# Performance work log

Measured on AMD Instinct MI355X. Metric: run time of the kernel, lower is better.

## Reference

```python
import jax, jax.numpy as jnp
import numpy as np

NUM_HEADS = 12
WS = 8
ROPE_BASE = 100.0  # croco/dust3r RoPE2D default frequency base


def _rope1d(t, p, inv_freq):
    # t: [Bw, h, N, d], p: [Bw, N], inv_freq: [d/2]
    freqs = p[..., None] * inv_freq                      # [Bw, N, d/2]
    emb = jnp.concatenate([freqs, freqs], axis=-1)       # [Bw, N, d]
    cos = jnp.cos(emb)[:, None, :, :]
    sin = jnp.sin(emb)[:, None, :, :]
    t1, t2 = jnp.split(t, 2, axis=-1)
    rot = jnp.concatenate([-t2, t1], axis=-1)            # rotate_half
    return t * cos + rot * sin


def _rope2d(tokens, pos):
    # tokens: [Bw, h, N, D], pos: [Bw, N, 2] (y, x). First D/2 dims use y, last D/2 use x.
    D = tokens.shape[-1]
    d = D // 2
    inv_freq = 1.0 / (ROPE_BASE ** (jnp.arange(0, d, 2, dtype=jnp.float32) / d))
    ty, tx = jnp.split(tokens, 2, axis=-1)
    return jnp.concatenate([_rope1d(ty, pos[..., 0], inv_freq),
                            _rope1d(tx, pos[..., 1], inv_freq)], axis=-1)


def setup_inputs() -> dict:
    B, H, W, C = 16, 64, 64, 768
    key = jax.random.key(0)
    ks = jax.random.split(key, 7)
    x_img = jax.random.normal(ks[0], (B, H * W, C), dtype=jnp.float32)
    yy, xx = jnp.meshgrid(jnp.arange(H), jnp.arange(W), indexing='ij')
    pos = jnp.stack([yy, xx], axis=-1).reshape(1, H * W, 2).astype(jnp.float32)
    pos2d_img = jnp.broadcast_to(pos, (B, H * W, 2))
    unseen = jax.random.normal(ks[1], (B, C), dtype=jnp.float32)
    sc = C ** -0.5
    qkv_w = jax.random.normal(ks[2], (3 * C, C), dtype=jnp.float32) * sc
    qkv_b = jax.random.normal(ks[3], (3 * C,), dtype=jnp.float32) * 0.02
    proj_w = jax.random.normal(ks[4], (C, C), dtype=jnp.float32) * sc
    proj_b = jax.random.normal(ks[5], (C,), dtype=jnp.float32) * 0.02
    return {'x_img': x_img, 'pos2d_img': pos2d_img, 'unseen': unseen,
            'qkv_w': qkv_w, 'qkv_b': qkv_b, 'proj_w': proj_w, 'proj_b': proj_b,
            'H': H, 'W': W}


def reference(x_img, pos2d_img, unseen, qkv_w, qkv_b, proj_w, proj_b, H, W):
    B, HW, C = x_img.shape
    hd = C // NUM_HEADS
    scale = hd ** -0.5
    nWh, nWw = H // WS, W // WS
    Bwin, Nwin = B * nWh * nWw, WS * WS

    # window partition
    xw = x_img.reshape(B, nWh, WS, nWw, WS, C).transpose(0, 1, 3, 2, 4, 5).reshape(Bwin, Nwin, C)
    pw = pos2d_img.reshape(B, nWh, WS, nWw, WS, 2).transpose(0, 1, 3, 2, 4, 5).reshape(Bwin, Nwin, 2)

    # append unseen token (shared across windows of an image)
    u = jnp.broadcast_to(unseen[:, None, None, :], (B, nWh * nWw, 1, C)).reshape(Bwin, 1, C)
    xw = jnp.concatenate([xw, u], axis=1)                # [Bwin, Nwin+1, C]

    qkv = xw @ qkv_w.T + qkv_b                           # [Bwin, N, 3C]
    qkv = qkv.reshape(Bwin, Nwin + 1, 3, NUM_HEADS, hd)
    q = qkv[:, :, 0].transpose(0, 2, 1, 3)               # [Bwin, h, N, hd]
    k = qkv[:, :, 1].transpose(0, 2, 1, 3)
    v = qkv[:, :, 2].transpose(0, 2, 1, 3)

    # RoPE2D on image tokens only; unseen token gets no RoPE
    q = jnp.concatenate([_rope2d(q[:, :, :Nwin], pw), q[:, :, Nwin:]], axis=2)
    k = jnp.concatenate([_rope2d(k[:, :, :Nwin], pw), k[:, :, Nwin:]], axis=2)

    attn = jax.nn.softmax(jnp.einsum('bhqd,bhkd->bhqk', q, k) * scale, axis=-1)
    out = jnp.einsum('bhqk,bhkd->bhqd', attn, v)
    out = out.transpose(0, 2, 1, 3).reshape(Bwin, Nwin + 1, C)
    out = out @ proj_w.T + proj_b

    # window merge
    out_img = out[:, :Nwin].reshape(B, nWh, nWw, WS, WS, C).transpose(0, 1, 3, 2, 4, 5).reshape(B, HW, C)
    out_unseen = out[:, Nwin].reshape(B, nWh * nWw, C).mean(axis=1)  # [B, C]
    return out_img, out_unseen
```

## Files before the change

kernel.cpp:

```cpp
#include <hip/hip_runtime.h>
#include <cstdint>
#include <cstddef>

typedef __attribute__((ext_vector_type(8)))  __bf16 bf16x8;
typedef __attribute__((ext_vector_type(4)))  float  f32x4;
typedef __attribute__((ext_vector_type(2)))  unsigned int u32x2;
typedef __attribute__((ext_vector_type(4)))  unsigned int u32x4;

#define DI __device__ __forceinline__

constexpr int Cdim = 768;
constexpr int C3   = 2304;
constexpr int NT   = 65;
constexpr int ROWS = 1024 * NT;
constexpr int ROWS_PAD = ROWS + 32;
constexpr int TP   = 96;
constexpr int PS   = 128;
constexpr long long OUT_IMG = 16LL * 4096 * 768;

DI float bf2f(unsigned short u) { unsigned int x = (unsigned int)u << 16; float f; __builtin_memcpy(&f, &x, 4); return f; }
DI unsigned short f2bf(float f) { unsigned int x; __builtin_memcpy(&x, &f, 4); x = x + 0x7fffu + ((x >> 16) & 1u); return (unsigned short)(x >> 16); }

DI void gload_lds16(const unsigned short* g, unsigned short* l) {
  __builtin_amdgcn_global_load_lds((__attribute__((address_space(1))) void*)g,
                                   (__attribute__((address_space(3))) void*)l, 16, 0, 0);
}

__global__ void k_prep(const float* __restrict__ qkv_w, const float* __restrict__ proj_w,
                       unsigned short* __restrict__ wqb, unsigned short* __restrict__ wpb,
                       float* __restrict__ rope) {
  const int NW1 = 2304 * 768;
  const int NW2 = 768 * 768;
  int total = NW1 + NW2 + 1024;
  for (int i = blockIdx.x * blockDim.x + threadIdx.x; i < total; i += gridDim.x * blockDim.x) {
    if (i < NW1) wqb[i] = f2bf(qkv_w[i]);
    else if (i < NW1 + NW2) wpb[i - NW1] = f2bf(proj_w[i - NW1]);
    else {
      int e = i - NW1 - NW2;
      int p = e >> 4, j = e & 15;
      float inv = powf(100.f, -(float)j * (1.f / 16.f));
      float a = (float)p * inv;
      rope[2 * e]     = cosf(a);
      rope[2 * e + 1] = sinf(a);
    }
  }
}

__global__ void k_xw(const float* __restrict__ x, const float* __restrict__ unseen,
                     unsigned short* __restrict__ xw) {
  int row = blockIdx.x;
  int w = row / NT, t = row - w * NT;
  const float* src;
  if (t == 64) {
    src = unseen + (size_t)(w >> 6) * Cdim;
  } else {
    int wy = (w >> 3) & 7, wx = w & 7;
    int hw = ((wy << 3) + (t >> 3)) * 64 + (wx << 3) + (t & 7);
    src = x + ((size_t)(w >> 6) * 4096 + hw) * Cdim;
  }
  float4 v = ((const float4*)src)[threadIdx.x];
  unsigned int u0 = (unsigned)f2bf(v.x) | ((unsigned)f2bf(v.y) << 16);
  unsigned int u1 = (unsigned)f2bf(v.z) | ((unsigned)f2bf(v.w) << 16);
  ((u32x2*)(xw + (size_t)row * Cdim))[threadIdx.x] = (u32x2){u0, u1};
}

template<int MODE, int NTILES>
__global__ __launch_bounds__(256, 4) void k_gemm(
    const unsigned short* __restrict__ A, const unsigned short* __restrict__ Bw,
    const float* __restrict__ bias, const float* __restrict__ rope,
    unsigned short* __restrict__ Cb, float* __restrict__ outp) {
  constexpr int K = 768;
  __shared__ alignas(16) unsigned short As[128 * 64];
  __shared__ alignas(16) unsigned short Bs[128 * 64];

  constexpr int nwg = 520 * NTILES;
  constexpr int q8 = nwg / 8, r8 = nwg % 8;
  int id = blockIdx.x;
  int xcd = id & 7, lid = id >> 3;
  int wg = (xcd < r8 ? xcd * (q8 + 1) : r8 * (q8 + 1) + (xcd - r8) * q8) + lid;
  int mtile = wg / NTILES, ntile = wg - mtile * NTILES;
  int m0 = mtile * 128, n0 = ntile * 128;

  int tid = threadIdx.x;
  int lane = tid & 63, wid = tid >> 6;
  int lq = lane & 15, lg = lane >> 4;
  int wm = (wid >> 1) * 64;
  int wn = (wid & 1) * 64;

  f32x4 acc[4][4];
  #pragma unroll
  for (int i = 0; i < 4; ++i)
    #pragma unroll
    for (int j = 0; j < 4; ++j) acc[i][j] = (f32x4){0.f, 0.f, 0.f, 0.f};

  for (int kt = 0; kt < K / 64; ++kt) {
    int k0 = kt * 64;
    #pragma unroll
    for (int c = 0; c < 4; ++c) {
      int chunk = c * 256 + tid;
      int row = chunk >> 3, kc = chunk & 7;
      int skc = kc ^ (row & 7);
      gload_lds16(A + (size_t)(m0 + row) * K + k0 + skc * 8,
                  As + (size_t)(c * 256 + (tid & ~63)) * 8);
    }
    #pragma unroll
    for (int c = 0; c < 4; ++c) {
      int chunk = c * 256 + tid;
      int row = chunk >> 3, kc = chunk & 7;
      int skc = kc ^ (row & 7);
      gload_lds16(Bw + (size_t)(n0 + row) * K + k0 + skc * 8,
                  Bs + (size_t)(c * 256 + (tid & ~63)) * 8);
    }
    asm volatile("s_waitcnt vmcnt(0)" ::: "memory");
    __syncthreads();
    #pragma unroll
    for (int ks = 0; ks < 2; ++ks) {
      bf16x8 af[4], bfr[4];
      #pragma unroll
      for (int mt = 0; mt < 4; ++mt) {
        int row = wm + mt * 16 + lq;
        int ch = ((ks << 2) + lg) ^ (row & 7);
        af[mt] = *(const bf16x8*)(As + row * 64 + ch * 8);
      }
      #pragma unroll
      for (int nt = 0; nt < 4; ++nt) {
        int row = wn + nt * 16 + lq;
        int ch = ((ks << 2) + lg) ^ (row & 7);
        bfr[nt] = *(const bf16x8*)(Bs + row * 64 + ch * 8);
      }
      #pragma unroll
      for (int mt = 0; mt < 4; ++mt)
        #pragma unroll
        for (int nt = 0; nt < 4; ++nt)
          acc[mt][nt] = __builtin_amdgcn_mfma_f32_16x16x32_bf16(af[mt], bfr[nt], acc[mt][nt], 0, 0, 0);
    }
    __syncthreads();
  }

  if (MODE == 0) {
    unsigned short* ct = As;
    #pragma unroll
    for (int mt = 0; mt < 4; ++mt) {
      #pragma unroll
      for (int r = 0; r < 4; ++r) {
        int lrow = wm + mt * 16 + (lg << 2) + r;
        int grow = m0 + lrow;
        int w = grow / NT, t = grow - w * NT;
        int wy = (w >> 3) & 7, wx = w & 7;
        int py = (wy << 3) + (t >> 3), px = (wx << 3) + (t & 7);
        #pragma unroll
        for (int a = 0; a < 2; ++a) {
          int cn0 = wn + a * 32 + lq;
          int col0 = n0 + cn0, col1 = col0 + 16;
          float v0 = acc[mt][2 * a][r] + bias[col0];
          float v1 = acc[mt][2 * a + 1][r] + bias[col1];
          if (col0 < 1536 && t != 64) {
            int p = a ? px : py;
            const float* rp = rope + ((p << 4) + lq) * 2;
            float cc = rp[0], ss = rp[1];
            float o0 = v0 * cc - v1 * ss;
            float o1 = v1 * cc + v0 * ss;
            v0 = o0; v1 = o1;
          }
          int b0 = (lrow * 256 + cn0 * 2) ^ ((lrow & 7) << 4);
          int b1 = (lrow * 256 + (cn0 + 16) * 2) ^ ((lrow & 7) << 4);
          *(unsigned short*)((char*)ct + b0) = f2bf(v0);
          *(unsigned short*)((char*)ct + b1) = f2bf(v1);
        }
      }
    }
    __syncthreads();
    #pragma unroll
    for (int j = 0; j < 8; ++j) {
      int idx = j * 256 + tid;
      int row = idx >> 4, c = idx & 15;
      u32x4 v = *(const u32x4*)((char*)ct + row * 256 + ((c ^ (row & 7)) << 4));
      *(u32x4*)(Cb + (size_t)(m0 + row) * C3 + n0 + c * 8) = v;
    }
  } else {
    float* cf = (float*)As;
    #pragma unroll
    for (int half = 0; half < 2; ++half) {
      if ((wm >> 6) == half) {
        #pragma unroll
        for (int mt = 0; mt < 4; ++mt) {
          #pragma unroll
          for (int r = 0; r < 4; ++r) {
            int lrow = mt * 16 + (lg << 2) + r;
            int grow = m0 + half * 64 + lrow;
            int w = grow / NT, t = grow - w * NT;
            #pragma unroll
            for (int a = 0; a < 2; ++a) {
              int cn0 = wn + a * 32 + lq;
              int col0 = n0 + cn0, col1 = col0 + 16;
              float v0 = acc[mt][2 * a][r] + bias[col0];
              float v1 = acc[mt][2 * a + 1][r] + bias[col1];
              if (t == 64) {
                float* ub = outp + OUT_IMG + (size_t)(w >> 6) * Cdim;
                atomicAdd(ub + col0, v0 * (1.f / 64.f));
                atomicAdd(ub + col1, v1 * (1.f / 64.f));
              } else {
                int b0 = (lrow * 512 + cn0 * 4) ^ ((lrow & 7) << 4);
                int b1 = (lrow * 512 + (cn0 + 16) * 4) ^ ((lrow & 7) << 4);
                *(float*)((char*)cf + b0) = v0;
                *(float*)((char*)cf + b1) = v1;
              }
            }
          }
        }
      }
      __syncthreads();
      #pragma unroll
      for (int j = 0; j < 8; ++j) {
        int idx = j * 256 + tid;
        int row = idx >> 5, c = idx & 31;
        int grow = m0 + half * 64 + row;
        int w = grow / NT, t = grow - w * NT;
        if (t != 64) {
          int wy = (w >> 3) & 7, wx = w & 7;
          int py = (wy << 3) + (t >> 3), px = (wx << 3) + (t & 7);
          u32x4 v = *(const u32x4*)((char*)cf + row * 512 + ((c ^ (row & 7)) << 4));
          *(u32x4*)(outp + ((size_t)(w >> 6) * 4096 + py * 64 + px) * Cdim + n0 + c * 4) = v;
        }
      }
      __syncthreads();
    }
  }
}

__global__ void k_vt(const unsigned short* __restrict__ qkv, unsigned short* __restrict__ Vt) {
  int bh = blockIdx.x;
  int w = bh / 12, h = bh - w * 12;
  __shared__ float sv[65][65];
  const unsigned short* base = qkv + (size_t)w * NT * C3 + 1536 + h * 64;
  for (int i = threadIdx.x; i < 65 * 64; i += 256) {
    int t = i >> 6, d = i & 63;
    sv[t][d] = bf2f(base[(size_t)t * C3 + d]);
  }
  __syncthreads();
  unsigned short* out = Vt + (size_t)bh * 64 * TP;
  for (int i = threadIdx.x; i < 64 * (TP / 8); i += 256) {
    int d = i / (TP / 8), tc = i - d * (TP / 8);
    int t0 = tc * 8;
    unsigned int u[4];
    #pragma unroll
    for (int k = 0; k < 4; ++k) {
      int ta = t0 + 2 * k, tb = ta + 1;
      unsigned short sa = (ta < 65) ? f2bf(sv[ta][d]) : (unsigned short)0;
      unsigned short sb = (tb < 65) ? f2bf(sv[tb][d]) : (unsigned short)0;
      u[k] = (unsigned)sa | ((unsigned)sb << 16);
    }
    *(u32x4*)(out + d * TP + t0) = (u32x4){u[0], u[1], u[2], u[3]};
  }
}

__global__ __launch_bounds__(64) void k_attn(const unsigned short* __restrict__ qkv,
                                             const unsigned short* __restrict__ Vt,
                                             unsigned short* __restrict__ att) {
  __shared__ alignas(16) unsigned short P[80 * PS];
  int h = blockIdx.x, w = blockIdx.y;
  int lane = threadIdx.x;
  int lq = lane & 15, lg = lane >> 4;

  const unsigned short* qb = qkv + (size_t)w * NT * C3 + h * 64;
  const unsigned short* kb = qb + 768;

  bf16x8 kf[5][2];
  #pragma unroll
  for (int kt = 0; kt < 5; ++kt)
    #pragma unroll
    for (int ks = 0; ks < 2; ++ks)
      kf[kt][ks] = *(const bf16x8*)(kb + (size_t)(kt * 16 + lq) * C3 + ks * 32 + lg * 8);

  const unsigned short* vb = Vt + (size_t)(w * 12 + h) * 64 * TP;
  bf16x8 vf[3][4];
  #pragma unroll
  for (int ks = 0; ks < 3; ++ks)
    #pragma unroll
    for (int dt = 0; dt < 4; ++dt)
      vf[ks][dt] = *(const bf16x8*)(vb + (size_t)(dt * 16 + lq) * TP + ks * 32 + lg * 8);

  for (int i = lane; i < 80 * 8; i += 64) {
    int row = i >> 3, j = i & 7;
    int byteo = row * (PS * 2) + 160 + j * 4;
    byteo ^= (row & 7) << 4;
    *(unsigned int*)((char*)P + byteo) = 0u;
  }

  #pragma unroll 1
  for (int qt = 0; qt < 5; ++qt) {
    bf16x8 qf[2];
    #pragma unroll
    for (int ks = 0; ks < 2; ++ks)
      qf[ks] = *(const bf16x8*)(qb + (size_t)(qt * 16 + lq) * C3 + ks * 32 + lg * 8);

    f32x4 sa[5];
    #pragma unroll
    for (int kt = 0; kt < 5; ++kt) {
      sa[kt] = (f32x4){0.f, 0.f, 0.f, 0.f};
      #pragma unroll
      for (int ks = 0; ks < 2; ++ks)
        sa[kt] = __builtin_amdgcn_mfma_f32_16x16x32_bf16(kf[kt][ks], qf[ks], sa[kt], 0, 0, 0);
    }
    float pv[5][4];
    float m = -1e30f;
    #pragma unroll
    for (int kt = 0; kt < 5; ++kt)
      #pragma unroll
      for (int r = 0; r < 4; ++r) {
        int tok = kt * 16 + lg * 4 + r;
        float s = sa[kt][r] * 0.125f;
        bool ok = tok < 65;
        pv[kt][r] = ok ? s : -1e30f;
        m = (ok && s > m) ? s : m;
      }
    m = fmaxf(m, __shfl_xor(m, 16));
    m = fmaxf(m, __shfl_xor(m, 32));
    float sum = 0.f;
    #pragma unroll
    for (int kt = 0; kt < 5; ++kt)
      #pragma unroll
      for (int r = 0; r < 4; ++r) {
        float e = (pv[kt][r] > -1e29f) ? exp2f((pv[kt][r] - m) * 1.44269504f) : 0.f;
        pv[kt][r] = e;
        sum += e;
      }
    sum += __shfl_xor(sum, 16);
    sum += __shfl_xor(sum, 32);
    float rinv = 1.f / sum;

    int q = qt * 16 + lq;
    #pragma unroll
    for (int kt = 0; kt < 5; ++kt) {
      unsigned int u0 = (unsigned)f2bf(pv[kt][0] * rinv) | ((unsigned)f2bf(pv[kt][1] * rinv) << 16);
      unsigned int u1 = (unsigned)f2bf(pv[kt][2] * rinv) | ((unsigned)f2bf(pv[kt][3] * rinv) << 16);
      int byteo = q * (PS * 2) + kt * 32 + lg * 8;
      byteo ^= (q & 7) << 4;
      *(u32x2*)((char*)P + byteo) = (u32x2){u0, u1};
    }
    asm volatile("s_waitcnt lgkmcnt(0)" ::: "memory");

    bf16x8 bp[3];
    #pragma unroll
    for (int ks = 0; ks < 3; ++ks) {
      int byteo = q * (PS * 2) + ks * 64 + lg * 16;
      byteo ^= (q & 7) << 4;
      bp[ks] = *(const bf16x8*)((char*)P + byteo);
    }
    #pragma unroll
    for (int dt = 0; dt < 4; ++dt) {
      f32x4 o = (f32x4){0.f, 0.f, 0.f, 0.f};
      #pragma unroll
      for (int ks = 0; ks < 3; ++ks)
        o = __builtin_amdgcn_mfma_f32_16x16x32_bf16(vf[ks][dt], bp[ks], o, 0, 0, 0);
      if (q < 65) {
        unsigned int u0 = (unsigned)f2bf(o[0]) | ((unsigned)f2bf(o[1]) << 16);
        unsigned int u1 = (unsigned)f2bf(o[2]) | ((unsigned)f2bf(o[3]) << 16);
        *(u32x2*)(att + (size_t)(w * NT + q) * Cdim + h * 64 + dt * 16 + lg * 4) = (u32x2){u0, u1};
      }
    }
  }
}

extern "C" void kernel_launch(void* const* d_in, const int* in_sizes, int n_in,
                              void* d_out, int out_size, void* d_ws, size_t ws_size,
                              hipStream_t stream) {
  const float* x_img  = (const float*)d_in[0];
  const float* unseen = (const float*)d_in[2];
  const float* qkv_w  = (const float*)d_in[3];
  const float* qkv_b  = (const float*)d_in[4];
  const float* proj_w = (const float*)d_in[5];
  const float* proj_b = (const float*)d_in[6];

  char* ws = (char*)d_ws;
  size_t off = 0;
  auto alloc = [&](size_t bytes) { void* p = ws + off; off = (off + bytes + 255) & ~(size_t)255; return p; };
  unsigned short* xw  = (unsigned short*)alloc((size_t)ROWS * Cdim * 2);
  unsigned short* qkv = (unsigned short*)alloc((size_t)ROWS_PAD * C3 * 2);
  unsigned short* Vt  = (unsigned short*)alloc((size_t)12288 * 64 * TP * 2);
  unsigned short* wqb = (unsigned short*)alloc((size_t)C3 * Cdim * 2);
  unsigned short* wpb = (unsigned short*)alloc((size_t)Cdim * Cdim * 2);
  float* rope = (float*)alloc(64 * 16 * 2 * sizeof(float));

  hipMemsetAsync((float*)d_out + OUT_IMG, 0, 16 * Cdim * sizeof(float), stream);

  k_prep<<<512, 256, 0, stream>>>(qkv_w, proj_w, wqb, wpb, rope);
  k_xw<<<ROWS, 192, 0, stream>>>(x_img, unseen, xw);
  k_gemm<0, 18><<<520 * 18, 256, 0, stream>>>(xw, wqb, qkv_b, rope, qkv, nullptr);
  k_vt<<<12288, 256, 0, stream>>>(qkv, Vt);
  k_attn<<<dim3(12, 1024), 64, 0, stream>>>(qkv, Vt, xw);
  k_gemm<1, 6><<<520 * 6, 256, 0, stream>>>(xw, wpb, proj_b, nullptr, nullptr, (float*)d_out);
}
```

Baseline: 658.0 us.

## Fuse V transpose into QKV GEMM epilogue and drop separate transpose kernel

The QKV GEMM epilogue now writes V-column tiles straight into the transposed, padded Vt layout from the LDS staging buffer, instead of storing them to the qkv buffer. The standalone k_vt kernel, which re-read V and wrote Vt, is removed. This saves a full round trip of V through global memory and one kernel launch, at the cost of a more irregular, partly scalar scatter in the epilogue for tiles that straddle window boundaries. Two smaller changes come with it: the attention kernel's P staging buffer shrinks to one 16-row tile reused per query tile, and the projection GEMM gets a higher min-waves launch bound. The Vt padding columns 65..95 are no longer written explicitly, so the code relies on that memory already being clean.

Result: slower. 805.5 us (+22.4%).

```diff
diff --git a/kernel.cpp b/kernel.cpp
--- a/kernel.cpp
+++ b/kernel.cpp
@@ -64,14 +64,16 @@
   ((u32x2*)(xw + (size_t)row * Cdim))[threadIdx.x] = (u32x2){u0, u1};
 }
 
-template<int MODE, int NTILES>
-__global__ __launch_bounds__(256, 4) void k_gemm(
+template<int MODE, int NTILES, int MW>
+__global__ __launch_bounds__(256, MW) void k_gemm(
     const unsigned short* __restrict__ A, const unsigned short* __restrict__ Bw,
     const float* __restrict__ bias, const float* __restrict__ rope,
-    unsigned short* __restrict__ Cb, float* __restrict__ outp) {
+    unsigned short* __restrict__ Cb, unsigned short* __restrict__ Vt,
+    float* __restrict__ outp) {
   constexpr int K = 768;
-  __shared__ alignas(16) unsigned short As[128 * 64];
-  __shared__ alignas(16) unsigned short Bs[128 * 64];
+  __shared__ alignas(16) unsigned short lds[16384];
+  unsigned short* As = lds;
+  unsigned short* Bs = lds + 8192;
 
   constexpr int nwg = 520 * NTILES;
   constexpr int q8 = nwg / 8, r8 = nwg % 8;
@@ -138,7 +140,7 @@
   }
 
   if (MODE == 0) {
-    unsigned short* ct = As;
+    unsigned short* ct = lds;
     #pragma unroll
     for (int mt = 0; mt < 4; ++mt) {
       #pragma unroll
@@ -170,15 +172,52 @@
       }
     }
     __syncthreads();
-    #pragma unroll
-    for (int j = 0; j < 8; ++j) {
-      int idx = j * 256 + tid;
-      int row = idx >> 4, c = idx & 15;
-      u32x4 v = *(const u32x4*)((char*)ct + row * 256 + ((c ^ (row & 7)) << 4));
-      *(u32x4*)(Cb + (size_t)(m0 + row) * C3 + n0 + c * 8) = v;
+    if (n0 < 1536) {
+      #pragma unroll
+      for (int j = 0; j < 8; ++j) {
+        int idx = j * 256 + tid;
+        int row = idx >> 4, c = idx & 15;
+        u32x4 v = *(const u32x4*)((char*)ct + row * 256 + ((c ^ (row & 7)) << 4));
+        *(u32x4*)(Cb + (size_t)(m0 + row) * C3 + n0 + c * 8) = v;
+      }
+    } else {
+      int w0 = m0 / NT;
+      int nwin = (m0 + 127) / NT - w0 + 1;
+      int nitems = nwin * 9 * 128;
+      for (int item = tid; item < nitems; item += 256) {
+        int c   = item & 127;
+        int rst = item >> 7;
+        int oc  = rst % 9;
+        int w   = w0 + rst / 9;
+        int tA = m0 - w * NT; if (tA < 0) tA = 0;
+        int tB = m0 + 128 - w * NT; if (tB > NT) tB = NT;
+        int t0 = oc * 8;
+        int a = t0 > tA ? t0 : tA;
+        int b = t0 + 8 < tB ? t0 + 8 : tB;
+        if (a >= b) continue;
+        int vc = n0 - 1536 + c;
+        unsigned short* vrow = Vt + (((size_t)w * 12 + (vc >> 6)) * 64 + (vc & 63)) * TP;
+        if (a == t0 && b == t0 + 8) {
+          unsigned int u[4];
+          #pragma unroll
+          for (int k = 0; k < 4; ++k) {
+            int ra = w * NT + t0 + 2 * k - m0;
+            int rb = ra + 1;
+            unsigned short va = *(const unsigned short*)((char*)ct + ((ra * 256 + c * 2) ^ ((ra & 7) << 4)));
+            unsigned short vb = *(const unsigned short*)((char*)ct + ((rb * 256 + c * 2) ^ ((rb & 7) << 4)));
+            u[k] = (unsigned)va | ((unsigned)vb << 16);
+          }
+          *(u32x4*)(vrow + t0) = (u32x4){u[0], u[1], u[2], u[3]};
+        } else {
+          for (int t = a; t < b; ++t) {
+            int r = w * NT + t - m0;
+            vrow[t] = *(const unsigned short*)((char*)ct + ((r * 256 + c * 2) ^ ((r & 7) << 4)));
+          }
+        }
+      }
     }
   } else {
-    float* cf = (float*)As;
+    float* cf = (float*)lds;
     #pragma unroll
     for (int half = 0; half < 2; ++half) {
       if ((wm >> 6) == half) {
@@ -228,36 +267,10 @@
   }
 }
 
-__global__ void k_vt(const unsigned short* __restrict__ qkv, unsigned short* __restrict__ Vt) {
-  int bh = blockIdx.x;
-  int w = bh / 12, h = bh - w * 12;
-  __shared__ float sv[65][65];
-  const unsigned short* base = qkv + (size_t)w * NT * C3 + 1536 + h * 64;
-  for (int i = threadIdx.x; i < 65 * 64; i += 256) {
-    int t = i >> 6, d = i & 63;
-    sv[t][d] = bf2f(base[(size_t)t * C3 + d]);
-  }
-  __syncthreads();
-  unsigned short* out = Vt + (size_t)bh * 64 * TP;
-  for (int i = threadIdx.x; i < 64 * (TP / 8); i += 256) {
-    int d = i / (TP / 8), tc = i - d * (TP / 8);
-    int t0 = tc * 8;
-    unsigned int u[4];
-    #pragma unroll
-    for (int k = 0; k < 4; ++k) {
-      int ta = t0 + 2 * k, tb = ta + 1;
-      unsigned short sa = (ta < 65) ? f2bf(sv[ta][d]) : (unsigned short)0;
-      unsigned short sb = (tb < 65) ? f2bf(sv[tb][d]) : (unsigned short)0;
-      u[k] = (unsigned)sa | ((unsigned)sb << 16);
-    }
-    *(u32x4*)(out + d * TP + t0) = (u32x4){u[0], u[1], u[2], u[3]};
-  }
-}
-
 __global__ __launch_bounds__(64) void k_attn(const unsigned short* __restrict__ qkv,
                                              const unsigned short* __restrict__ Vt,
                                              unsigned short* __restrict__ att) {
-  __shared__ alignas(16) unsigned short P[80 * PS];
+  __shared__ alignas(16) unsigned short P[16 * PS];
   int h = blockIdx.x, w = blockIdx.y;
   int lane = threadIdx.x;
   int lq = lane & 15, lg = lane >> 4;
@@ -280,10 +293,9 @@
     for (int dt = 0; dt < 4; ++dt)
       vf[ks][dt] = *(const bf16x8*)(vb + (size_t)(dt * 16 + lq) * TP + ks * 32 + lg * 8);
 
-  for (int i = lane; i < 80 * 8; i += 64) {
+  for (int i = lane; i < 16 * 8; i += 64) {
     int row = i >> 3, j = i & 7;
-    int byteo = row * (PS * 2) + 160 + j * 4;
-    byteo ^= (row & 7) << 4;
+    int byteo = (row * (PS * 2) + 160 + j * 4) ^ ((row & 7) << 4);
     *(unsigned int*)((char*)P + byteo) = 0u;
   }
 
@@ -334,8 +346,7 @@
     for (int kt = 0; kt < 5; ++kt) {
       unsigned int u0 = (unsigned)f2bf(pv[kt][0] * rinv) | ((unsigned)f2bf(pv[kt][1] * rinv) << 16);
       unsigned int u1 = (unsigned)f2bf(pv[kt][2] * rinv) | ((unsigned)f2bf(pv[kt][3] * rinv) << 16);
-      int byteo = q * (PS * 2) + kt * 32 + lg * 8;
-      byteo ^= (q & 7) << 4;
+      int byteo = (lq * (PS * 2) + kt * 32 + lg * 8) ^ ((lq & 7) << 4);
       *(u32x2*)((char*)P + byteo) = (u32x2){u0, u1};
     }
     asm volatile("s_waitcnt lgkmcnt(0)" ::: "memory");
@@ -343,8 +354,7 @@
     bf16x8 bp[3];
     #pragma unroll
     for (int ks = 0; ks < 3; ++ks) {
-      int byteo = q * (PS * 2) + ks * 64 + lg * 16;
-      byteo ^= (q & 7) << 4;
+      int byteo = (lq * (PS * 2) + ks * 64 + lg * 16) ^ ((lq & 7) << 4);
       bp[ks] = *(const bf16x8*)((char*)P + byteo);
     }
     #pragma unroll
@@ -386,8 +396,7 @@
 
   k_prep<<<512, 256, 0, stream>>>(qkv_w, proj_w, wqb, wpb, rope);
   k_xw<<<ROWS, 192, 0, stream>>>(x_img, unseen, xw);
-  k_gemm<0, 18><<<520 * 18, 256, 0, stream>>>(xw, wqb, qkv_b, rope, qkv, nullptr);
-  k_vt<<<12288, 256, 0, stream>>>(qkv, Vt);
+  k_gemm<0, 18, 4><<<520 * 18, 256, 0, stream>>>(xw, wqb, qkv_b, rope, qkv, Vt, nullptr);
   k_attn<<<dim3(12, 1024), 64, 0, stream>>>(qkv, Vt, xw);
-  k_gemm<1, 6><<<520 * 6, 256, 0, stream>>>(xw, wpb, proj_b, nullptr, nullptr, (float*)d_out);
-}
+  k_gemm<1, 6, 5><<<520 * 6, 256, 0, stream>>>(xw, wpb, proj_b, nullptr, nullptr, nullptr, (float*)d_out);
+}
```
